# Kernel optimization log

Measured on AMD Instinct MI355X. Metric: run time of the kernel, lower is better.

The kernel has to match this reference:

```python
import math
import jax, jax.numpy as jnp
import numpy as np

EMBED_SIZE = 1024
NUM_HEADS = 16
HEAD_DIM = EMBED_SIZE // NUM_HEADS
N, L = 8, 1024
MASK_FILL = -1e3  # value used by masked_fill in the original (NOT -inf)
SCALE = 1.0 / math.sqrt(EMBED_SIZE)  # original divides by embed_size**0.5, not head_dim


def setup_inputs() -> dict:
    key = jax.random.key(0)
    ks = jax.random.split(key, 7)
    values = jax.random.normal(ks[0], (N, L, EMBED_SIZE), dtype=jnp.float32)
    keys_t = jax.random.normal(ks[1], (N, L, EMBED_SIZE), dtype=jnp.float32)
    queries = jax.random.normal(ks[2], (N, L, EMBED_SIZE), dtype=jnp.float32)
    attn_mask = jax.random.randint(ks[3], (1, 1, L, L), 0, 2, dtype=jnp.int32)
    scr_key_padding_mask = jax.random.randint(ks[4], (N, 1, 1, L), 0, 2, dtype=jnp.int32)
    # fc_out: nn.Linear(embed_size, embed_size) with bias
    fc_w = jax.random.normal(ks[5], (EMBED_SIZE, EMBED_SIZE), dtype=jnp.float32) * (1.0 / math.sqrt(EMBED_SIZE))
    fc_b = jax.random.normal(ks[6], (EMBED_SIZE,), dtype=jnp.float32) * 0.01
    return {"values": values, "keys": keys_t, "queries": queries,
            "fc_w": fc_w, "fc_b": fc_b,
            "attn_mask": attn_mask, "scr_key_padding_mask": scr_key_padding_mask}


def reference(values, keys, queries, fc_w, fc_b, attn_mask, scr_key_padding_mask):
    n, q_len, e = queries.shape
    k_len = keys.shape[1]
    h, d = NUM_HEADS, HEAD_DIM
    # NOTE: the original defines per-head Linear projections but never applies them
    v = values.reshape(n, k_len, h, d)
    k = keys.reshape(n, k_len, h, d)
    q = queries.reshape(n, q_len, h, d)
    energy = jnp.einsum('nqhd,nkhd->nhqk', q, k)  # [n, h, q, k]
    am = attn_mask[:, :, :k_len, :k_len]
    energy = jnp.where(am == 0, MASK_FILL, energy)
    energy = jnp.where(scr_key_padding_mask == 0, MASK_FILL, energy)
    attention = jax.nn.softmax(energy * SCALE, axis=3)
    out = jnp.einsum('nhql,nlhd->nqhd', attention, v).reshape(n, q_len, h * d)
    return out @ fc_w.T + fc_b
```

## Files before the change

kernel.cpp:

```cpp
#include <hip/hip_runtime.h>

#define L_SEQ 1024
#define EMB 1024
#define NH 16
#define HD 64

typedef _Float16 half8 __attribute__((ext_vector_type(8)));
typedef _Float16 half4v __attribute__((ext_vector_type(4)));
typedef __fp16 h2 __attribute__((ext_vector_type(2)));
typedef float f32x4 __attribute__((ext_vector_type(4)));
typedef float fvec4 __attribute__((ext_vector_type(4)));
typedef unsigned int u32;
typedef unsigned long long u64;

constexpr float C2 = 0.045084220027780106f;

constexpr int FP = 40;
constexpr int PP = 72;

__device__ __forceinline__ void async16(const void* g, void* l) {
    __builtin_amdgcn_global_load_lds((const __attribute__((address_space(1))) u32*)g,
                                     (__attribute__((address_space(3))) u32*)l, 16, 0, 0);
}

__global__ void pack_mask_kernel(const int* __restrict__ am, u32* __restrict__ bits,
                                 const int* __restrict__ pad, u32* __restrict__ pbits) {
    const int i = blockIdx.x * 256 + threadIdx.x;
    const int lane = threadIdx.x & 63;
    u64 b = __ballot(am[i] != 0);
    if (lane == 0)       bits[i >> 5] = (u32)b;
    else if (lane == 32) bits[i >> 5] = (u32)(b >> 32);
    if (blockIdx.x < 32) {
        const int j = blockIdx.x * 256 + threadIdx.x;
        u64 pb = __ballot(pad[j] != 0);
        if (lane == 0)       pbits[j >> 5] = (u32)pb;
        else if (lane == 32) pbits[j >> 5] = (u32)(pb >> 32);
    }
}

__global__ void convert_w_kernel(const float* __restrict__ w, _Float16* __restrict__ o) {
    size_t i = ((size_t)blockIdx.x * blockDim.x + threadIdx.x) * 4;
    fvec4 v = *(const fvec4*)(w + i);
    half4v h;
#pragma unroll
    for (int j = 0; j < 4; ++j) h[j] = (_Float16)v[j];
    *(half4v*)(o + i) = h;
}

__global__ __launch_bounds__(256) void cvt_kv_kernel(
    const float* __restrict__ keys, const float* __restrict__ values,
    _Float16* __restrict__ K16, _Float16* __restrict__ Vt16)
{
    __shared__ __align__(16) _Float16 Vt[64 * PP];
    const int tid = threadIdx.x;
    const int kt = blockIdx.x, h = blockIdx.y, n = blockIdx.z;
    const int kbase = kt * 64;
    const int r = tid >> 2, c0 = (tid & 3) * 16;
    const int nh = n * NH + h;

    {
        const float* src = keys + ((size_t)(n * L_SEQ + kbase + r)) * EMB + h * HD + c0;
        fvec4 a0 = *(const fvec4*)(src),     a1 = *(const fvec4*)(src + 4);
        fvec4 a2 = *(const fvec4*)(src + 8), a3 = *(const fvec4*)(src + 12);
        half8 o0, o1;
#pragma unroll
        for (int j = 0; j < 4; ++j) {
            o0[j] = (_Float16)(a0[j] * C2); o0[j + 4] = (_Float16)(a1[j] * C2);
            o1[j] = (_Float16)(a2[j] * C2); o1[j + 4] = (_Float16)(a3[j] * C2);
        }
        _Float16* dst = K16 + ((size_t)nh * L_SEQ + kbase + r) * HD + c0;
        *(half8*)dst = o0; *(half8*)(dst + 8) = o1;
    }
    {
        const float* src = values + ((size_t)(n * L_SEQ + kbase + r)) * EMB + h * HD + c0;
        fvec4 vv[4];
        vv[0] = *(const fvec4*)(src);     vv[1] = *(const fvec4*)(src + 4);
        vv[2] = *(const fvec4*)(src + 8); vv[3] = *(const fvec4*)(src + 12);
#pragma unroll
        for (int i = 0; i < 16; ++i)
            Vt[(c0 + i) * PP + r] = (_Float16)vv[i >> 2][i & 3];
    }
    __syncthreads();
    {
        const int d = tid >> 2, k0 = (tid & 3) * 16;
        half8 v0 = *(const half8*)(&Vt[d * PP + k0]);
        half8 v1 = *(const half8*)(&Vt[d * PP + k0 + 8]);
        _Float16* dst = Vt16 + ((size_t)nh * HD + d) * L_SEQ + kbase + k0;
        *(half8*)dst = v0; *(half8*)(dst + 8) = v1;
    }
}

__global__ __launch_bounds__(256, 3) void attn_kernel(
    const _Float16* __restrict__ K16, const _Float16* __restrict__ Vt16,
    const float* __restrict__ queries, const u32* __restrict__ mbits,
    const u32* __restrict__ pbits, _Float16* __restrict__ out_f16)
{
    __shared__ __align__(16) _Float16 K_lds[2][64 * 64];
    __shared__ __align__(16) _Float16 V_lds[2][64 * 64];
    __shared__ __align__(16) _Float16 P_lds[128 * PP];
    __shared__ __align__(8)  u32 mtab[32];

    const int tid  = threadIdx.x;
    const int lane = tid & 63;
    const int wave = tid >> 6;
    const int l16  = lane & 15;
    const int quad = lane >> 4;
    const int bid  = blockIdx.x;
    const int nh = bid & 127, qt = bid >> 7;
    const int n = nh >> 4, h = nh & 15;
    const int qbase = qt * 128;
    const int xr = l16 & 7;
    const int quad4 = quad * 4;

    const _Float16* Kt_base = K16 + (size_t)nh * L_SEQ * HD;
    const _Float16* Vt_base = Vt16 + (size_t)nh * HD * L_SEQ;
    const int gch = (lane & 7) ^ ((lane >> 3) & 7);

    auto stage = [&](int buf, int kt) {
        const int kbase = kt * 64;
#pragma unroll
        for (int s2 = 0; s2 < 2; ++s2) {
            const int row = wave * 16 + s2 * 8 + (lane >> 3);
            async16(Kt_base + (size_t)(kbase + row) * HD + gch * 8,
                    &K_lds[buf][(wave * 16 + s2 * 8) * 64]);
            async16(Vt_base + (size_t)row * L_SEQ + kbase + gch * 8,
                    &V_lds[buf][(wave * 16 + s2 * 8) * 64]);
        }
    };

    stage(0, 0);

    if (tid < 16) {
        mtab[tid * 2]     = ((tid & 1) ? 0x3C00u : 0u) | ((tid & 2) ? 0x3C000000u : 0u);
        mtab[tid * 2 + 1] = ((tid & 4) ? 0x3C00u : 0u) | ((tid & 8) ? 0x3C000000u : 0u);
    }

    half8 qf[2][2];
#pragma unroll
    for (int s = 0; s < 2; ++s) {
        const int qrow = qbase + wave * 32 + s * 16 + l16;
        const float* qp = queries + ((size_t)(n * L_SEQ + qrow)) * EMB + h * HD;
#pragma unroll
        for (int t = 0; t < 2; ++t) {
            fvec4 a = *(const fvec4*)(qp + t * 32 + quad * 8);
            fvec4 b = *(const fvec4*)(qp + t * 32 + quad * 8 + 4);
#pragma unroll
            for (int j = 0; j < 4; ++j) { qf[s][t][j] = (_Float16)a[j]; qf[s][t][j + 4] = (_Float16)b[j]; }
        }
    }

    f32x4 Ov[2][4];
#pragma unroll
    for (int s = 0; s < 2; ++s)
#pragma unroll
        for (int dt = 0; dt < 4; ++dt) Ov[s][dt] = (f32x4){0.f, 0.f, 0.f, 0.f};
    float lsum[2] = {0.f, 0.f};
    const h2 one2 = {(__fp16)1.f, (__fp16)1.f};

    int cur = 0;
#pragma unroll 2
    for (int kt = 0; kt < L_SEQ / 64; ++kt) {
        __syncthreads();
        if (kt + 1 < L_SEQ / 64) stage(cur ^ 1, kt + 1);

        uint2 wm[2];
#pragma unroll
        for (int s = 0; s < 2; ++s) {
            const int qrow = qbase + wave * 32 + s * 16 + l16;
            wm[s] = *(const uint2*)(&mbits[qrow * 32 + kt * 2]);
        }
        const u32 plo = pbits[(n << 5) + (kt << 1)];
        const u32 phi = pbits[(n << 5) + (kt << 1) + 1];

        f32x4 S[2][4];
#pragma unroll
        for (int s = 0; s < 2; ++s)
#pragma unroll
            for (int tj = 0; tj < 4; ++tj) S[s][tj] = (f32x4){0.f, 0.f, 0.f, 0.f};

        const _Float16* kb = &K_lds[cur][0];
#pragma unroll
        for (int tj = 0; tj < 4; ++tj) {
            const _Float16* kr = kb + (tj * 16 + l16) * 64;
            const int c0 = (quad ^ xr) * 8;
            half8 k0 = *(const half8*)(kr + c0);
            half8 k1 = *(const half8*)(kr + (c0 ^ 32));
            S[0][tj] = __builtin_amdgcn_mfma_f32_16x16x32_f16(k0, qf[0][0], S[0][tj], 0, 0, 0);
            S[0][tj] = __builtin_amdgcn_mfma_f32_16x16x32_f16(k1, qf[0][1], S[0][tj], 0, 0, 0);
            S[1][tj] = __builtin_amdgcn_mfma_f32_16x16x32_f16(k0, qf[1][0], S[1][tj], 0, 0, 0);
            S[1][tj] = __builtin_amdgcn_mfma_f32_16x16x32_f16(k1, qf[1][1], S[1][tj], 0, 0, 0);
        }

#pragma unroll
        for (int s = 0; s < 2; ++s) {
            const u32 pw0 = wm[s].x & plo, pw1 = wm[s].y & phi;
#pragma unroll
            for (int tj = 0; tj < 4; ++tj) {
                const u32 m4 = (((tj & 2) ? pw1 : pw0) >> ((tj & 1) * 16 + quad4)) & 15u;
                const uint2 mm = *(const uint2*)(&mtab[m4 * 2]);
                const float p0 = __builtin_amdgcn_exp2f(S[s][tj][0]);
                const float p1 = __builtin_amdgcn_exp2f(S[s][tj][1]);
                const float p2 = __builtin_amdgcn_exp2f(S[s][tj][2]);
                const float p3 = __builtin_amdgcn_exp2f(S[s][tj][3]);
                const h2 q01 = __builtin_amdgcn_cvt_pkrtz(p0, p1) * __builtin_bit_cast(h2, mm.x);
                const h2 q23 = __builtin_amdgcn_cvt_pkrtz(p2, p3) * __builtin_bit_cast(h2, mm.y);
                lsum[s] = __builtin_amdgcn_fdot2(q01, one2, lsum[s], false);
                lsum[s] = __builtin_amdgcn_fdot2(q23, one2, lsum[s], false);
                uint2 st;
                st.x = __builtin_bit_cast(u32, q01);
                st.y = __builtin_bit_cast(u32, q23);
                *(uint2*)(&P_lds[(wave * 32 + s * 16 + l16) * PP + tj * 16 + quad4]) = st;
            }
        }

        const _Float16* vb = &V_lds[cur][0];
        half8 pf0[2], pf1[2];
#pragma unroll
        for (int t = 0; t < 2; ++t) {
            pf0[t] = *(const half8*)(&P_lds[(wave * 32 + l16) * PP + t * 32 + quad * 8]);
            pf1[t] = *(const half8*)(&P_lds[(wave * 32 + 16 + l16) * PP + t * 32 + quad * 8]);
        }
#pragma unroll
        for (int t = 0; t < 2; ++t) {
            const int c0 = ((t * 4 + quad) ^ xr) * 8;
#pragma unroll
            for (int dt = 0; dt < 4; ++dt) {
                half8 vf = *(const half8*)(&vb[(dt * 16 + l16) * 64 + c0]);
                Ov[0][dt] = __builtin_amdgcn_mfma_f32_16x16x32_f16(pf0[t], vf, Ov[0][dt], 0, 0, 0);
                Ov[1][dt] = __builtin_amdgcn_mfma_f32_16x16x32_f16(pf1[t], vf, Ov[1][dt], 0, 0, 0);
            }
        }
        cur ^= 1;
    }

#pragma unroll
    for (int s = 0; s < 2; ++s) {
        lsum[s] += __shfl_xor(lsum[s], 16);
        lsum[s] += __shfl_xor(lsum[s], 32);
    }
#pragma unroll
    for (int s = 0; s < 2; ++s)
#pragma unroll
        for (int reg = 0; reg < 4; ++reg) {
            const float linv = 1.0f / fmaxf(__shfl(lsum[s], quad4 + reg), 1e-25f);
            const int qrow = qbase + wave * 32 + s * 16 + quad4 + reg;
            _Float16* op = out_f16 + ((size_t)(n * L_SEQ + qrow)) * EMB + h * HD;
#pragma unroll
            for (int dt = 0; dt < 4; ++dt)
                op[dt * 16 + l16] = (_Float16)(Ov[s][dt][reg] * linv);
        }
}

__global__ __launch_bounds__(256) void fc_kernel(
    const _Float16* __restrict__ A, const _Float16* __restrict__ W,
    const float* __restrict__ bias, float* __restrict__ C)
{
    __shared__ __align__(16) _Float16 As[128 * FP];
    __shared__ __align__(16) _Float16 Ws[128 * FP];

    const int tid = threadIdx.x;
    const int lane = tid & 63;
    const int wv = tid >> 6;
    const int l16 = lane & 15;
    const int quad = lane >> 4;
    const int wm = (wv >> 1) * 64, wn = (wv & 1) * 64;
    const int Mb = blockIdx.x * 128, Nb = blockIdx.y * 128;

    f32x4 acc[4][4];
#pragma unroll
    for (int i = 0; i < 4; ++i)
#pragma unroll
        for (int j = 0; j < 4; ++j) acc[i][j] = (f32x4){0.f, 0.f, 0.f, 0.f};

    for (int k0 = 0; k0 < EMB; k0 += 32) {
        __syncthreads();
#pragma unroll
        for (int s = 0; s < 2; ++s) {
            const int id = tid + s * 256;
            const int row = id >> 2, ch = (id & 3) * 8;
            *(half8*)(&As[row * FP + ch]) = *(const half8*)(A + (size_t)(Mb + row) * EMB + k0 + ch);
            *(half8*)(&Ws[row * FP + ch]) = *(const half8*)(W + (size_t)(Nb + row) * EMB + k0 + ch);
        }
        __syncthreads();

        half8 af[4], bf[4];
#pragma unroll
        for (int i = 0; i < 4; ++i) {
            af[i] = *(const half8*)(&As[(wm + i * 16 + l16) * FP + quad * 8]);
            bf[i] = *(const half8*)(&Ws[(wn + i * 16 + l16) * FP + quad * 8]);
        }
#pragma unroll
        for (int i = 0; i < 4; ++i)
#pragma unroll
            for (int j = 0; j < 4; ++j)
                acc[i][j] = __builtin_amdgcn_mfma_f32_16x16x32_f16(af[i], bf[j], acc[i][j], 0, 0, 0);
    }

#pragma unroll
    for (int i = 0; i < 4; ++i) {
        const int m = Mb + wm + i * 16 + quad * 4;
#pragma unroll
        for (int j = 0; j < 4; ++j) {
            const int jc = Nb + wn + j * 16 + l16;
            const float b = bias[jc];
#pragma unroll
            for (int reg = 0; reg < 4; ++reg)
                C[(size_t)(m + reg) * EMB + jc] = acc[i][j][reg] + b;
        }
    }
}

extern "C" void kernel_launch(void* const* d_in, const int* in_sizes, int n_in,
                              void* d_out, int out_size, void* d_ws, size_t ws_size,
                              hipStream_t stream) {
    const float* values  = (const float*)d_in[0];
    const float* keys    = (const float*)d_in[1];
    const float* queries = (const float*)d_in[2];
    const float* fc_w    = (const float*)d_in[3];
    const float* fc_b    = (const float*)d_in[4];
    const int*   amask   = (const int*)d_in[5];
    const int*   pmask   = (const int*)d_in[6];
    float* out = (float*)d_out;

    char* w = (char*)d_ws;
    _Float16* attn_out = (_Float16*)w;
    _Float16* w_f16    = (_Float16*)(w + (size_t)16 * 1024 * 1024);
    u32*      mbits    = (u32*)(w + (size_t)18 * 1024 * 1024);
    u32*      pbits    = (u32*)(w + (size_t)18 * 1024 * 1024 + 128 * 1024);
    _Float16* K16      = (_Float16*)(w + (size_t)19 * 1024 * 1024);
    _Float16* Vt16     = (_Float16*)(w + (size_t)35 * 1024 * 1024);

    pack_mask_kernel<<<4096, 256, 0, stream>>>(amask, mbits, pmask, pbits);
    convert_w_kernel<<<1024, 256, 0, stream>>>(fc_w, w_f16);
    cvt_kv_kernel<<<dim3(16, 16, 8), 256, 0, stream>>>(keys, values, K16, Vt16);
    attn_kernel<<<1024, 256, 0, stream>>>(K16, Vt16, queries, mbits, pbits, attn_out);
    fc_kernel<<<dim3(64, 8), 256, 0, stream>>>(attn_out, w_f16, fc_b, out);
}
```

Baseline: 235.7 us.

## Switch attention to 32x32x16 MFMA and keep P in registers via permlane32 swap

The attention kernel now computes S^T and O with 32x32x16 MFMA tiles instead of 16x16x32. Each wave handles 32 query rows, one per lane pair. The P shared-memory round trip is removed: probabilities are rearranged in registers with v_permlane32_swap so they feed directly as the MFMA operand for the PV product. s_setprio hints are also added around the MFMA blocks. This removes LDS writes and reads plus their latency, and lowers LDS usage, at the cost of larger accumulator register pressure and a layout change whose correctness relies on the permlane32 swap mapping.

```diff
diff --git a/kernel.cpp b/kernel.cpp
--- a/kernel.cpp
+++ b/kernel.cpp
@@ -9,8 +9,10 @@
 typedef _Float16 half4v __attribute__((ext_vector_type(4)));
 typedef __fp16 h2 __attribute__((ext_vector_type(2)));
 typedef float f32x4 __attribute__((ext_vector_type(4)));
+typedef float f32x16 __attribute__((ext_vector_type(16)));
 typedef float fvec4 __attribute__((ext_vector_type(4)));
 typedef unsigned int u32;
+typedef u32 u32x4 __attribute__((ext_vector_type(4)));
 typedef unsigned long long u64;
 
 constexpr float C2 = 0.045084220027780106f;
@@ -97,20 +99,19 @@
 {
     __shared__ __align__(16) _Float16 K_lds[2][64 * 64];
     __shared__ __align__(16) _Float16 V_lds[2][64 * 64];
-    __shared__ __align__(16) _Float16 P_lds[128 * PP];
     __shared__ __align__(8)  u32 mtab[32];
 
     const int tid  = threadIdx.x;
     const int lane = tid & 63;
-    const int wave = tid >> 6;
-    const int l16  = lane & 15;
-    const int quad = lane >> 4;
+    const int wv   = tid >> 6;
+    const int l32  = lane & 31;
+    const int hi   = lane >> 5;
     const int bid  = blockIdx.x;
     const int nh = bid & 127, qt = bid >> 7;
     const int n = nh >> 4, h = nh & 15;
     const int qbase = qt * 128;
-    const int xr = l16 & 7;
-    const int quad4 = quad * 4;
+    const int q = qbase + wv * 32 + l32;
+    const int rsw = l32 & 7;
 
     const _Float16* Kt_base = K16 + (size_t)nh * L_SEQ * HD;
     const _Float16* Vt_base = Vt16 + (size_t)nh * HD * L_SEQ;
@@ -120,11 +121,11 @@
         const int kbase = kt * 64;
 #pragma unroll
         for (int s2 = 0; s2 < 2; ++s2) {
-            const int row = wave * 16 + s2 * 8 + (lane >> 3);
+            const int row = wv * 16 + s2 * 8 + (lane >> 3);
             async16(Kt_base + (size_t)(kbase + row) * HD + gch * 8,
-                    &K_lds[buf][(wave * 16 + s2 * 8) * 64]);
+                    &K_lds[buf][(wv * 16 + s2 * 8) * 64]);
             async16(Vt_base + (size_t)row * L_SEQ + kbase + gch * 8,
-                    &V_lds[buf][(wave * 16 + s2 * 8) * 64]);
+                    &V_lds[buf][(wv * 16 + s2 * 8) * 64]);
         }
     };
 
@@ -135,26 +136,24 @@
         mtab[tid * 2 + 1] = ((tid & 4) ? 0x3C00u : 0u) | ((tid & 8) ? 0x3C000000u : 0u);
     }
 
-    half8 qf[2][2];
-#pragma unroll
-    for (int s = 0; s < 2; ++s) {
-        const int qrow = qbase + wave * 32 + s * 16 + l16;
-        const float* qp = queries + ((size_t)(n * L_SEQ + qrow)) * EMB + h * HD;
-#pragma unroll
-        for (int t = 0; t < 2; ++t) {
-            fvec4 a = *(const fvec4*)(qp + t * 32 + quad * 8);
-            fvec4 b = *(const fvec4*)(qp + t * 32 + quad * 8 + 4);
-#pragma unroll
-            for (int j = 0; j < 4; ++j) { qf[s][t][j] = (_Float16)a[j]; qf[s][t][j + 4] = (_Float16)b[j]; }
-        }
-    }
-
-    f32x4 Ov[2][4];
-#pragma unroll
-    for (int s = 0; s < 2; ++s)
-#pragma unroll
-        for (int dt = 0; dt < 4; ++dt) Ov[s][dt] = (f32x4){0.f, 0.f, 0.f, 0.f};
-    float lsum[2] = {0.f, 0.f};
+    half8 qf[4];
+    {
+        const float* qp = queries + ((size_t)(n * L_SEQ + q)) * EMB + h * HD;
+#pragma unroll
+        for (int c = 0; c < 4; ++c) {
+            fvec4 a = *(const fvec4*)(qp + c * 16 + hi * 8);
+            fvec4 b = *(const fvec4*)(qp + c * 16 + hi * 8 + 4);
+#pragma unroll
+            for (int j = 0; j < 4; ++j) { qf[c][j] = (_Float16)a[j]; qf[c][j + 4] = (_Float16)b[j]; }
+        }
+    }
+
+    f32x16 Ov[2];
+#pragma unroll
+    for (int dt = 0; dt < 2; ++dt)
+#pragma unroll
+        for (int r = 0; r < 16; ++r) Ov[dt][r] = 0.f;
+    float lsum = 0.f;
     const h2 one2 = {(__fp16)1.f, (__fp16)1.f};
 
     int cur = 0;
@@ -163,92 +162,94 @@
         __syncthreads();
         if (kt + 1 < L_SEQ / 64) stage(cur ^ 1, kt + 1);
 
-        uint2 wm[2];
-#pragma unroll
-        for (int s = 0; s < 2; ++s) {
-            const int qrow = qbase + wave * 32 + s * 16 + l16;
-            wm[s] = *(const uint2*)(&mbits[qrow * 32 + kt * 2]);
-        }
-        const u32 plo = pbits[(n << 5) + (kt << 1)];
-        const u32 phi = pbits[(n << 5) + (kt << 1) + 1];
-
-        f32x4 S[2][4];
-#pragma unroll
-        for (int s = 0; s < 2; ++s)
-#pragma unroll
-            for (int tj = 0; tj < 4; ++tj) S[s][tj] = (f32x4){0.f, 0.f, 0.f, 0.f};
+        const uint2 wmq = *(const uint2*)(&mbits[(size_t)q * 32 + kt * 2]);
+        u32 w[2];
+        w[0] = wmq.x & pbits[(n << 5) + (kt << 1)];
+        w[1] = wmq.y & pbits[(n << 5) + (kt << 1) + 1];
+
+        f32x16 St[2];
+#pragma unroll
+        for (int i = 0; i < 2; ++i)
+#pragma unroll
+            for (int r = 0; r < 16; ++r) St[i][r] = 0.f;
 
         const _Float16* kb = &K_lds[cur][0];
-#pragma unroll
-        for (int tj = 0; tj < 4; ++tj) {
-            const _Float16* kr = kb + (tj * 16 + l16) * 64;
-            const int c0 = (quad ^ xr) * 8;
-            half8 k0 = *(const half8*)(kr + c0);
-            half8 k1 = *(const half8*)(kr + (c0 ^ 32));
-            S[0][tj] = __builtin_amdgcn_mfma_f32_16x16x32_f16(k0, qf[0][0], S[0][tj], 0, 0, 0);
-            S[0][tj] = __builtin_amdgcn_mfma_f32_16x16x32_f16(k1, qf[0][1], S[0][tj], 0, 0, 0);
-            S[1][tj] = __builtin_amdgcn_mfma_f32_16x16x32_f16(k0, qf[1][0], S[1][tj], 0, 0, 0);
-            S[1][tj] = __builtin_amdgcn_mfma_f32_16x16x32_f16(k1, qf[1][1], S[1][tj], 0, 0, 0);
-        }
-
-#pragma unroll
-        for (int s = 0; s < 2; ++s) {
-            const u32 pw0 = wm[s].x & plo, pw1 = wm[s].y & phi;
-#pragma unroll
-            for (int tj = 0; tj < 4; ++tj) {
-                const u32 m4 = (((tj & 2) ? pw1 : pw0) >> ((tj & 1) * 16 + quad4)) & 15u;
-                const uint2 mm = *(const uint2*)(&mtab[m4 * 2]);
-                const float p0 = __builtin_amdgcn_exp2f(S[s][tj][0]);
-                const float p1 = __builtin_amdgcn_exp2f(S[s][tj][1]);
-                const float p2 = __builtin_amdgcn_exp2f(S[s][tj][2]);
-                const float p3 = __builtin_amdgcn_exp2f(S[s][tj][3]);
-                const h2 q01 = __builtin_amdgcn_cvt_pkrtz(p0, p1) * __builtin_bit_cast(h2, mm.x);
-                const h2 q23 = __builtin_amdgcn_cvt_pkrtz(p2, p3) * __builtin_bit_cast(h2, mm.y);
-                lsum[s] = __builtin_amdgcn_fdot2(q01, one2, lsum[s], false);
-                lsum[s] = __builtin_amdgcn_fdot2(q23, one2, lsum[s], false);
-                uint2 st;
-                st.x = __builtin_bit_cast(u32, q01);
-                st.y = __builtin_bit_cast(u32, q23);
-                *(uint2*)(&P_lds[(wave * 32 + s * 16 + l16) * PP + tj * 16 + quad4]) = st;
+        __builtin_amdgcn_s_setprio(1);
+#pragma unroll
+        for (int c = 0; c < 4; ++c) {
+            const int ch = ((2 * c + hi) ^ rsw) * 8;
+            half8 kf0 = *(const half8*)(kb + l32 * 64 + ch);
+            half8 kf1 = *(const half8*)(kb + (32 + l32) * 64 + ch);
+            St[0] = __builtin_amdgcn_mfma_f32_32x32x16_f16(kf0, qf[c], St[0], 0, 0, 0);
+            St[1] = __builtin_amdgcn_mfma_f32_32x32x16_f16(kf1, qf[c], St[1], 0, 0, 0);
+        }
+        __builtin_amdgcn_s_setprio(0);
+
+        u32 pa[4][4];
+#pragma unroll
+        for (int i = 0; i < 2; ++i) {
+#pragma unroll
+            for (int rgp = 0; rgp < 2; ++rgp) {
+                const int rg_a = 2 * rgp, rg_b = 2 * rgp + 1;
+                const u32 m4a = (w[i] >> (8 * rg_a + 4 * hi)) & 15u;
+                const u32 m4b = (w[i] >> (8 * rg_b + 4 * hi)) & 15u;
+                const uint2 mma = *(const uint2*)(&mtab[m4a * 2]);
+                const uint2 mmb = *(const uint2*)(&mtab[m4b * 2]);
+                const float pa0 = __builtin_amdgcn_exp2f(St[i][4 * rg_a + 0]);
+                const float pa1 = __builtin_amdgcn_exp2f(St[i][4 * rg_a + 1]);
+                const float pa2 = __builtin_amdgcn_exp2f(St[i][4 * rg_a + 2]);
+                const float pa3 = __builtin_amdgcn_exp2f(St[i][4 * rg_a + 3]);
+                const float pb0 = __builtin_amdgcn_exp2f(St[i][4 * rg_b + 0]);
+                const float pb1 = __builtin_amdgcn_exp2f(St[i][4 * rg_b + 1]);
+                const float pb2 = __builtin_amdgcn_exp2f(St[i][4 * rg_b + 2]);
+                const float pb3 = __builtin_amdgcn_exp2f(St[i][4 * rg_b + 3]);
+                const h2 a0 = __builtin_amdgcn_cvt_pkrtz(pa0, pa1) * __builtin_bit_cast(h2, mma.x);
+                const h2 a1 = __builtin_amdgcn_cvt_pkrtz(pa2, pa3) * __builtin_bit_cast(h2, mma.y);
+                const h2 b0 = __builtin_amdgcn_cvt_pkrtz(pb0, pb1) * __builtin_bit_cast(h2, mmb.x);
+                const h2 b1 = __builtin_amdgcn_cvt_pkrtz(pb2, pb3) * __builtin_bit_cast(h2, mmb.y);
+                lsum = __builtin_amdgcn_fdot2(a0, one2, lsum, false);
+                lsum = __builtin_amdgcn_fdot2(a1, one2, lsum, false);
+                lsum = __builtin_amdgcn_fdot2(b0, one2, lsum, false);
+                lsum = __builtin_amdgcn_fdot2(b1, one2, lsum, false);
+                u32 A0 = __builtin_bit_cast(u32, a0), A1 = __builtin_bit_cast(u32, a1);
+                u32 B0 = __builtin_bit_cast(u32, b0), B1 = __builtin_bit_cast(u32, b1);
+                asm("v_permlane32_swap_b32 %0, %1" : "+v"(A0), "+v"(B0));
+                asm("v_permlane32_swap_b32 %0, %1" : "+v"(A1), "+v"(B1));
+                const int ks = i * 2 + rgp;
+                pa[ks][0] = A0; pa[ks][1] = A1; pa[ks][2] = B0; pa[ks][3] = B1;
             }
         }
 
         const _Float16* vb = &V_lds[cur][0];
-        half8 pf0[2], pf1[2];
-#pragma unroll
-        for (int t = 0; t < 2; ++t) {
-            pf0[t] = *(const half8*)(&P_lds[(wave * 32 + l16) * PP + t * 32 + quad * 8]);
-            pf1[t] = *(const half8*)(&P_lds[(wave * 32 + 16 + l16) * PP + t * 32 + quad * 8]);
-        }
-#pragma unroll
-        for (int t = 0; t < 2; ++t) {
-            const int c0 = ((t * 4 + quad) ^ xr) * 8;
-#pragma unroll
-            for (int dt = 0; dt < 4; ++dt) {
-                half8 vf = *(const half8*)(&vb[(dt * 16 + l16) * 64 + c0]);
-                Ov[0][dt] = __builtin_amdgcn_mfma_f32_16x16x32_f16(pf0[t], vf, Ov[0][dt], 0, 0, 0);
-                Ov[1][dt] = __builtin_amdgcn_mfma_f32_16x16x32_f16(pf1[t], vf, Ov[1][dt], 0, 0, 0);
-            }
-        }
+        __builtin_amdgcn_s_setprio(1);
+#pragma unroll
+        for (int ks = 0; ks < 4; ++ks) {
+            u32x4 pw = {pa[ks][0], pa[ks][1], pa[ks][2], pa[ks][3]};
+            half8 pB = __builtin_bit_cast(half8, pw);
+            const int ch = ((2 * ks + hi) ^ rsw) * 8;
+            half8 vf0 = *(const half8*)(vb + l32 * 64 + ch);
+            half8 vf1 = *(const half8*)(vb + (32 + l32) * 64 + ch);
+            Ov[0] = __builtin_amdgcn_mfma_f32_32x32x16_f16(pB, vf0, Ov[0], 0, 0, 0);
+            Ov[1] = __builtin_amdgcn_mfma_f32_32x32x16_f16(pB, vf1, Ov[1], 0, 0, 0);
+        }
+        __builtin_amdgcn_s_setprio(0);
         cur ^= 1;
     }
 
-#pragma unroll
-    for (int s = 0; s < 2; ++s) {
-        lsum[s] += __shfl_xor(lsum[s], 16);
-        lsum[s] += __shfl_xor(lsum[s], 32);
-    }
-#pragma unroll
-    for (int s = 0; s < 2; ++s)
-#pragma unroll
-        for (int reg = 0; reg < 4; ++reg) {
-            const float linv = 1.0f / fmaxf(__shfl(lsum[s], quad4 + reg), 1e-25f);
-            const int qrow = qbase + wave * 32 + s * 16 + quad4 + reg;
-            _Float16* op = out_f16 + ((size_t)(n * L_SEQ + qrow)) * EMB + h * HD;
-#pragma unroll
-            for (int dt = 0; dt < 4; ++dt)
-                op[dt * 16 + l16] = (_Float16)(Ov[s][dt][reg] * linv);
-        }
+    lsum += __shfl_xor(lsum, 32);
+    float linv[16];
+#pragma unroll
+    for (int reg = 0; reg < 16; ++reg) {
+        const int qrel = (reg & 3) + 8 * (reg >> 2) + 4 * hi;
+        linv[reg] = 1.0f / fmaxf(__shfl(lsum, qrel), 1e-25f);
+    }
+#pragma unroll
+    for (int reg = 0; reg < 16; ++reg) {
+        const int qrow = qbase + wv * 32 + (reg & 3) + 8 * (reg >> 2) + 4 * hi;
+        _Float16* op = out_f16 + ((size_t)(n * L_SEQ + qrow)) * EMB + h * HD;
+        op[l32]      = (_Float16)(Ov[0][reg] * linv[reg]);
+        op[32 + l32] = (_Float16)(Ov[1][reg] * linv[reg]);
+    }
 }
 
 __global__ __launch_bounds__(256) void fc_kernel(
```

After: 237.2 us. About the same (+0.6%).
